# Performance work log

Hardware: AMD Instinct MI355X
Metric: run time of the kernel (lower is better)

Reference implementation:

```python
import jax, jax.numpy as jnp
import numpy as np

N = 50000      # nodes
E = 800000     # edges (avg degree 16)
IN = 256       # in_features
F1 = 32        # gnn_features per head
F2 = 32        # out_features per head
H = 8          # heads
NEG_SLOPE = 0.2


def setup_inputs() -> dict:
    key = jax.random.key(0)
    ks = jax.random.split(key, 12)
    s = 0.05
    return {
        "x":   jax.random.normal(ks[0], (N, IN), jnp.float32),
        "W1":  jax.random.normal(ks[1], (IN, H * F1), jnp.float32) * s,
        "al1": jax.random.normal(ks[2], (H, F1), jnp.float32) * s,
        "ar1": jax.random.normal(ks[3], (H, F1), jnp.float32) * s,
        "b1":  jnp.zeros((H, F1), jnp.float32),
        "W2":  jax.random.normal(ks[4], (F1, H * F2), jnp.float32) * s,
        "al2": jax.random.normal(ks[5], (H, F2), jnp.float32) * s,
        "ar2": jax.random.normal(ks[6], (H, F2), jnp.float32) * s,
        "b2":  jnp.zeros((H, F2), jnp.float32),
        "src": jax.random.randint(ks[7], (E,), 0, N, jnp.int32),
        "dst": jax.random.randint(ks[8], (E,), 0, N, jnp.int32),
    }


def _gat_layer(x, W, al, ar, b, src, dst):
    """One DGL-style GATConv. x:[N,Fin] -> [N,H,F]."""
    n, h, f = x.shape[0], al.shape[0], al.shape[1]
    z = (x @ W).reshape(n, h, f)                      # [N,H,F] projected feats
    el = jnp.einsum('nhf,hf->nh', z, al)              # src attention logits
    er = jnp.einsum('nhf,hf->nh', z, ar)              # dst attention logits
    e = el[src] + er[dst]                             # [E,H]
    e = jnp.where(e >= 0, e, NEG_SLOPE * e)           # LeakyReLU(0.2)
    # segmented (per-destination) softmax over incoming edges
    m = jax.ops.segment_max(e, dst, num_segments=n)   # [N,H]
    ex = jnp.exp(e - m[dst])                          # [E,H]
    denom = jax.ops.segment_sum(ex, dst, num_segments=n)
    alpha = ex / denom[dst]                           # [E,H]
    # weighted scatter-aggregate
    out = jax.ops.segment_sum(alpha[:, :, None] * z[src], dst, num_segments=n)
    return out + b[None]                              # [N,H,F]


def reference(x, W1, al1, ar1, b1, W2, al2, ar2, b2, src, dst):
    h = _gat_layer(x, W1, al1, ar1, b1, src, dst).mean(axis=1)   # [N,F1]
    h = jax.nn.elu(h)                                            # Dropout(0.5) = identity in eval
    out = _gat_layer(h, W2, al2, ar2, b2, src, dst).mean(axis=1) # [N,F2]
    return out
```

## Files before the change

### kernel.cpp

```cpp
#include <hip/hip_runtime.h>
#include <hip/hip_fp16.h>
#include <math.h>

#define IN_F 256
#define NHEAD 8
#define FDIM 32
#define SCAN_B 512

typedef _Float16 f16x8 __attribute__((ext_vector_type(8)));
typedef float f32x4 __attribute__((ext_vector_type(4)));

__device__ inline unsigned pkh2(float x, float y) {
  __half2 h = __floats2half2_rn(x, y);
  return *reinterpret_cast<unsigned*>(&h);
}


__global__ __launch_bounds__(256) void hist_k(const int* __restrict__ dst,
                                              int* __restrict__ deg, int E) {
  int i = blockIdx.x * 256 + threadIdx.x;
  if (i < E) atomicAdd(&deg[dst[i]], 1);
}

__global__ __launch_bounds__(SCAN_B) void scan1_k(const int* __restrict__ deg,
                                                  int* __restrict__ offs,
                                                  int* __restrict__ bsum, int N) {
  __shared__ int s[SCAN_B];
  int t = threadIdx.x;
  int i = blockIdx.x * SCAN_B + t;
  s[t] = (i < N) ? deg[i] : 0;
  __syncthreads();
  for (int off = 1; off < SCAN_B; off <<= 1) {
    int add = (t >= off) ? s[t - off] : 0;
    __syncthreads();
    s[t] += add;
    __syncthreads();
  }
  if (i < N) offs[i + 1] = s[t];
  if (t == SCAN_B - 1) bsum[blockIdx.x] = s[t];
}

__global__ __launch_bounds__(SCAN_B) void scan2_k(int* __restrict__ bsum, int nb) {
  __shared__ int s[SCAN_B];
  int t = threadIdx.x;
  s[t] = (t < nb) ? bsum[t] : 0;
  __syncthreads();
  for (int off = 1; off < SCAN_B; off <<= 1) {
    int add = (t >= off) ? s[t - off] : 0;
    __syncthreads();
    s[t] += add;
    __syncthreads();
  }
  if (t < nb) bsum[t] = (t == 0) ? 0 : s[t - 1];
}

__global__ __launch_bounds__(SCAN_B) void scan3_k(int* __restrict__ offs,
                                                  const int* __restrict__ bsum, int N) {
  int i = blockIdx.x * SCAN_B + threadIdx.x;
  if (i < N) offs[i + 1] += bsum[blockIdx.x];
  if (i == 0) offs[0] = 0;
}

__global__ __launch_bounds__(256) void scatter_k(const int* __restrict__ src,
                                                 const int* __restrict__ dst,
                                                 const int* __restrict__ offs,
                                                 int* __restrict__ cursor,
                                                 int* __restrict__ esrc, int E) {
  int i = blockIdx.x * 256 + threadIdx.x;
  if (i < E) {
    int d = dst[i];
    int pos = offs[d] + atomicAdd(&cursor[d], 1);
    esrc[pos] = src[i];
  }
}

__global__ __launch_bounds__(256) void w1cvt_k(const float* __restrict__ W1,
                                               __half* __restrict__ W1t) {
  __shared__ float s[16][17];
  int bx = blockIdx.x * 16, by = blockIdx.y * 16;
  int tx = threadIdx.x, ty = threadIdx.y;
  s[ty][tx] = W1[(by + ty) * 256 + bx + tx];
  __syncthreads();
  W1t[(size_t)(bx + ty) * 256 + by + tx] = __float2half(s[tx][ty]);
}

__global__ __launch_bounds__(256) void gemm_xw_mfma_k(const float* __restrict__ X,
                                                      const __half* __restrict__ W1t,
                                                      __half* __restrict__ Zh, int M) {
  int t = threadIdx.x;
  int wv = t >> 6, l = t & 63;
  int r = l & 15, kg = l >> 4;
  int row0 = blockIdx.x * 64 + wv * 16;
  int row = row0 + r;
  int rowc = (row < M) ? row : (M - 1);

  f16x8 a[8];
  const float* xp = X + (size_t)rowc * 256 + kg * 8;
#pragma unroll
  for (int ks = 0; ks < 8; ++ks) {
    float4 f0 = *reinterpret_cast<const float4*>(xp + ks * 32);
    float4 f1 = *reinterpret_cast<const float4*>(xp + ks * 32 + 4);
    f16x8 av;
    av[0] = (_Float16)f0.x; av[1] = (_Float16)f0.y;
    av[2] = (_Float16)f0.z; av[3] = (_Float16)f0.w;
    av[4] = (_Float16)f1.x; av[5] = (_Float16)f1.y;
    av[6] = (_Float16)f1.z; av[7] = (_Float16)f1.w;
    a[ks] = av;
  }

#pragma unroll 4
  for (int nf = 0; nf < 16; ++nf) {
    int col = nf * 16 + r;
    const f16x8* bp = reinterpret_cast<const f16x8*>(W1t + (size_t)col * 256 + kg * 8);
    f32x4 acc = {0.f, 0.f, 0.f, 0.f};
#pragma unroll
    for (int ks = 0; ks < 8; ++ks) {
      f16x8 bv = bp[ks * 4];
      acc = __builtin_amdgcn_mfma_f32_16x16x32_f16(a[ks], bv, acc, 0, 0, 0);
    }
    int orow = row0 + kg * 4;
#pragma unroll
    for (int i = 0; i < 4; ++i) {
      if (orow + i < M)
        Zh[(size_t)(orow + i) * 256 + nf * 16 + r] = __float2half((float)acc[i]);
    }
  }
}

__global__ __launch_bounds__(256) void gemm_h_k(const float* __restrict__ Hmat,
                                                const float* __restrict__ W2,
                                                __half* __restrict__ Zh, int M) {
  __shared__ float Ws[32][256];
  __shared__ float Hs[32][20];
  int t = threadIdx.x;
  for (int i = t; i < 32 * 256; i += 256) Ws[i >> 8][i & 255] = W2[i];
  int row0 = blockIdx.x * 16;
  for (int i = t; i < 16 * 32; i += 256) {
    int r = i >> 5, k = i & 31;
    Hs[k][r] = (row0 + r < M) ? Hmat[(size_t)(row0 + r) * 32 + k] : 0.f;
  }
  __syncthreads();
  int tx = t & 63, ty = t >> 6;
  float acc[4][4] = {};
#pragma unroll
  for (int k = 0; k < 32; ++k) {
    float4 a4 = *reinterpret_cast<const float4*>(&Hs[k][ty * 4]);
    float4 b4 = *reinterpret_cast<const float4*>(&Ws[k][tx * 4]);
    float a[4] = {a4.x, a4.y, a4.z, a4.w};
    float b[4] = {b4.x, b4.y, b4.z, b4.w};
#pragma unroll
    for (int i = 0; i < 4; ++i)
#pragma unroll
      for (int j = 0; j < 4; ++j) acc[i][j] = fmaf(a[i], b[j], acc[i][j]);
  }
#pragma unroll
  for (int i = 0; i < 4; ++i) {
    int r = row0 + ty * 4 + i;
    if (r < M) {
      uint2 w;
      w.x = pkh2(acc[i][0], acc[i][1]);
      w.y = pkh2(acc[i][2], acc[i][3]);
      *reinterpret_cast<uint2*>(&Zh[(size_t)r * 256 + tx * 4]) = w;
    }
  }
}

__global__ __launch_bounds__(256) void logits_k(const __half* __restrict__ Zh,
                                                const float* __restrict__ al,
                                                const float* __restrict__ ar,
                                                float* __restrict__ el,
                                                float* __restrict__ er, int N) {
  int wave = threadIdx.x >> 6;
  int lane = threadIdx.x & 63;
  int n = blockIdx.x * 4 + wave;
  if (n >= N) return;
  uint2 u = *reinterpret_cast<const uint2*>(&Zh[(size_t)n * 256 + lane * 4]);
  float2 f0 = __half22float2(*reinterpret_cast<__half2*>(&u.x));
  float2 f1 = __half22float2(*reinterpret_cast<__half2*>(&u.y));
  float4 a4 = reinterpret_cast<const float4*>(al)[lane];
  float4 r4 = reinterpret_cast<const float4*>(ar)[lane];
  float pl = f0.x * a4.x + f0.y * a4.y + f1.x * a4.z + f1.y * a4.w;
  float pr = f0.x * r4.x + f0.y * r4.y + f1.x * r4.z + f1.y * r4.w;
  pl += __shfl_xor(pl, 1); pl += __shfl_xor(pl, 2); pl += __shfl_xor(pl, 4);
  pr += __shfl_xor(pr, 1); pr += __shfl_xor(pr, 2); pr += __shfl_xor(pr, 4);
  if ((lane & 7) == 0) {
    int h = lane >> 3;
    el[(size_t)n * 8 + h] = pl;
    er[(size_t)n * 8 + h] = pr;
  }
}

__global__ __launch_bounds__(256) void alpha_k(const float* __restrict__ el,
                                               const float* __restrict__ er,
                                               const int* __restrict__ offs,
                                               const int* __restrict__ esrc,
                                               float* __restrict__ alf,
                                               float* __restrict__ rden, int N) {
  int g = blockIdx.x * 256 + threadIdx.x;
  if (g >= N * NHEAD) return;
  int n = g >> 3, h = g & 7;
  int beg = offs[n], end = offs[n + 1];
  float er_h = er[g];
  float m = -INFINITY;
  for (int i = beg; i < end; ++i) {
    float e = el[(size_t)esrc[i] * 8 + h] + er_h;
    e = (e >= 0.f) ? e : 0.2f * e;
    m = fmaxf(m, e);
  }
  float s = 0.f;
  for (int i = beg; i < end; ++i) {
    float e = el[(size_t)esrc[i] * 8 + h] + er_h;
    e = (e >= 0.f) ? e : 0.2f * e;
    float ex = __expf(e - m);
    alf[(size_t)i * 8 + h] = ex;
    s += ex;
  }
  rden[g] = (end > beg) ? 1.f / s : 0.f;
}

template <bool LAYER1>
__global__ __launch_bounds__(256) void agg_k(const __half* __restrict__ Zh,
                                             const float* __restrict__ alf,
                                             const float* __restrict__ rden,
                                             const float* __restrict__ bias,
                                             const int* __restrict__ offs,
                                             const int* __restrict__ esrc,
                                             float* __restrict__ out, int N) {
  int wid = threadIdx.x >> 6, lane = threadIdx.x & 63;
  int n = blockIdx.x * 4 + wid;
  if (n >= N) return;
  int h = lane >> 3, q = lane & 7;
  int beg = offs[n], end = offs[n + 1];
  float4 acc = make_float4(0.f, 0.f, 0.f, 0.f);
#pragma unroll 4
  for (int i = beg; i < end; ++i) {
    int sidx = esrc[i];
    float a = alf[(size_t)i * 8 + h];
    uint2 u = *reinterpret_cast<const uint2*>(&Zh[(size_t)sidx * 256 + h * 32 + q * 4]);
    float2 f0 = __half22float2(*reinterpret_cast<__half2*>(&u.x));
    float2 f1 = __half22float2(*reinterpret_cast<__half2*>(&u.y));
    acc.x = fmaf(a, f0.x, acc.x);
    acc.y = fmaf(a, f0.y, acc.y);
    acc.z = fmaf(a, f1.x, acc.z);
    acc.w = fmaf(a, f1.y, acc.w);
  }
  float r = rden[(size_t)n * 8 + h];
  float4 b4 = *reinterpret_cast<const float4*>(&bias[h * 32 + q * 4]);
  float4 v;
  v.x = fmaf(acc.x, r, b4.x);
  v.y = fmaf(acc.y, r, b4.y);
  v.z = fmaf(acc.z, r, b4.z);
  v.w = fmaf(acc.w, r, b4.w);
#pragma unroll
  for (int off = 8; off < 64; off <<= 1) {
    v.x += __shfl_xor(v.x, off);
    v.y += __shfl_xor(v.y, off);
    v.z += __shfl_xor(v.z, off);
    v.w += __shfl_xor(v.w, off);
  }
  if (h == 0) {
    v.x *= 0.125f; v.y *= 0.125f; v.z *= 0.125f; v.w *= 0.125f;
    if (LAYER1) {
      v.x = (v.x > 0.f) ? v.x : expm1f(v.x);
      v.y = (v.y > 0.f) ? v.y : expm1f(v.y);
      v.z = (v.z > 0.f) ? v.z : expm1f(v.z);
      v.w = (v.w > 0.f) ? v.w : expm1f(v.w);
    }
    *reinterpret_cast<float4*>(&out[(size_t)n * 32 + q * 4]) = v;
  }
}


extern "C" void kernel_launch(void* const* d_in, const int* in_sizes, int n_in,
                              void* d_out, int out_size, void* d_ws, size_t ws_size,
                              hipStream_t stream) {
  const float* x   = (const float*)d_in[0];
  const float* W1  = (const float*)d_in[1];
  const float* al1 = (const float*)d_in[2];
  const float* ar1 = (const float*)d_in[3];
  const float* b1  = (const float*)d_in[4];
  const float* W2  = (const float*)d_in[5];
  const float* al2 = (const float*)d_in[6];
  const float* ar2 = (const float*)d_in[7];
  const float* b2  = (const float*)d_in[8];
  const int* src   = (const int*)d_in[9];
  const int* dst   = (const int*)d_in[10];
  float* out = (float*)d_out;

  const int N = in_sizes[0] / IN_F;
  const int E = in_sizes[9];

  char* p = (char*)d_ws;
  auto alloc = [&](size_t bytes) {
    char* q = p;
    p += (bytes + 255) & ~(size_t)255;
    return q;
  };
  __half* zh  = (__half*)alloc((size_t)N * 256 * 2);
  __half* w1t = (__half*)alloc((size_t)256 * 256 * 2);
  float* el   = (float*)alloc((size_t)N * 8 * 4);
  float* er   = (float*)alloc((size_t)N * 8 * 4);
  float* h1   = (float*)alloc((size_t)N * 32 * 4);
  float* alf  = (float*)alloc((size_t)E * 8 * 4);
  float* rden = (float*)alloc((size_t)N * 8 * 4);
  int* offs   = (int*)alloc((size_t)(N + 1) * 4);
  int* deg    = (int*)alloc((size_t)N * 4);
  int* cursor = (int*)alloc((size_t)N * 4);
  int* bsum   = (int*)alloc((size_t)SCAN_B * 4);
  int* esrc   = (int*)alloc((size_t)E * 4);

  hipMemsetAsync(deg, 0, (size_t)N * 4, stream);
  hipMemsetAsync(cursor, 0, (size_t)N * 4, stream);

  int nb = (N + SCAN_B - 1) / SCAN_B;
  hist_k<<<(E + 255) / 256, 256, 0, stream>>>(dst, deg, E);
  scan1_k<<<nb, SCAN_B, 0, stream>>>(deg, offs, bsum, N);
  scan2_k<<<1, SCAN_B, 0, stream>>>(bsum, nb);
  scan3_k<<<nb, SCAN_B, 0, stream>>>(offs, bsum, N);
  scatter_k<<<(E + 255) / 256, 256, 0, stream>>>(src, dst, offs, cursor, esrc, E);

  int nh_blocks = (N * NHEAD + 255) / 256;

  w1cvt_k<<<dim3(16, 16), dim3(16, 16), 0, stream>>>(W1, w1t);
  gemm_xw_mfma_k<<<(N + 63) / 64, 256, 0, stream>>>(x, w1t, zh, N);
  logits_k<<<(N + 3) / 4, 256, 0, stream>>>(zh, al1, ar1, el, er, N);
  alpha_k<<<nh_blocks, 256, 0, stream>>>(el, er, offs, esrc, alf, rden, N);
  agg_k<true><<<(N + 3) / 4, 256, 0, stream>>>(zh, alf, rden, b1, offs, esrc, h1, N);

  gemm_h_k<<<(N + 15) / 16, 256, 0, stream>>>(h1, W2, zh, N);
  logits_k<<<(N + 3) / 4, 256, 0, stream>>>(zh, al2, ar2, el, er, N);
  alpha_k<<<nh_blocks, 256, 0, stream>>>(el, er, offs, esrc, alf, rden, N);
  agg_k<false><<<(N + 3) / 4, 256, 0, stream>>>(zh, alf, rden, b2, offs, esrc, out, N);
}
```

Baseline: 483.0 us.

## Stage W1 in swizzled LDS and compute two row tiles per wave

The X·W1 GEMM now loads the whole 256x256 fp16 W1t into a 128KB LDS buffer with an XOR swizzle. Previously each wave read B fragments straight from global memory. Each wave now handles 32 rows (two 16-row A tiles), so every B fragment is reused twice, and it splits the K accumulation into two independent chains to expose more MFMA parallelism. Blocks grow to 512 threads covering 256 rows with one block per CU. The cost is lower occupancy and a per-block 128KB LDS fill that must finish before compute starts.

```diff
diff --git a/kernel.cpp b/kernel.cpp
--- a/kernel.cpp
+++ b/kernel.cpp
@@ -84,45 +84,101 @@
   W1t[(size_t)(bx + ty) * 256 + by + tx] = __float2half(s[tx][ty]);
 }
 
-__global__ __launch_bounds__(256) void gemm_xw_mfma_k(const float* __restrict__ X,
-                                                      const __half* __restrict__ W1t,
-                                                      __half* __restrict__ Zh, int M) {
+__global__ __launch_bounds__(512, 1) void gemm_xw_mfma_k(const float* __restrict__ X,
+                                                         const __half* __restrict__ W1t,
+                                                         __half* __restrict__ Zh, int M) {
+  __shared__ __half Ws[256 * 256];
   int t = threadIdx.x;
-  int wv = t >> 6, l = t & 63;
+
+#pragma unroll
+  for (int i = 0; i < 16; ++i) {
+    int chunk = t + i * 512;
+    int col = chunk >> 5;
+    int g = chunk & 31;
+    f16x8 v = *reinterpret_cast<const f16x8*>(W1t + (size_t)col * 256 + g * 8);
+    int gs = g ^ (col & 31);
+    *reinterpret_cast<f16x8*>(&Ws[col * 256 + gs * 8]) = v;
+  }
+
+  int wid = t >> 6, l = t & 63;
   int r = l & 15, kg = l >> 4;
-  int row0 = blockIdx.x * 64 + wv * 16;
-  int row = row0 + r;
-  int rowc = (row < M) ? row : (M - 1);
-
-  f16x8 a[8];
-  const float* xp = X + (size_t)rowc * 256 + kg * 8;
+  int row0 = blockIdx.x * 256 + wid * 32;
+
+  int rowA0 = row0 + r;
+  int rowA1 = row0 + 16 + r;
+  int rc0 = (rowA0 < M) ? rowA0 : (M - 1);
+  int rc1 = (rowA1 < M) ? rowA1 : (M - 1);
+  const float* xp0 = X + (size_t)rc0 * 256 + kg * 8;
+  const float* xp1 = X + (size_t)rc1 * 256 + kg * 8;
+  f16x8 a0[8], a1[8];
 #pragma unroll
   for (int ks = 0; ks < 8; ++ks) {
-    float4 f0 = *reinterpret_cast<const float4*>(xp + ks * 32);
-    float4 f1 = *reinterpret_cast<const float4*>(xp + ks * 32 + 4);
+    float4 f0 = *reinterpret_cast<const float4*>(xp0 + ks * 32);
+    float4 f1 = *reinterpret_cast<const float4*>(xp0 + ks * 32 + 4);
     f16x8 av;
     av[0] = (_Float16)f0.x; av[1] = (_Float16)f0.y;
     av[2] = (_Float16)f0.z; av[3] = (_Float16)f0.w;
     av[4] = (_Float16)f1.x; av[5] = (_Float16)f1.y;
     av[6] = (_Float16)f1.z; av[7] = (_Float16)f1.w;
-    a[ks] = av;
-  }
-
-#pragma unroll 4
+    a0[ks] = av;
+    float4 g0 = *reinterpret_cast<const float4*>(xp1 + ks * 32);
+    float4 g1 = *reinterpret_cast<const float4*>(xp1 + ks * 32 + 4);
+    f16x8 bv;
+    bv[0] = (_Float16)g0.x; bv[1] = (_Float16)g0.y;
+    bv[2] = (_Float16)g0.z; bv[3] = (_Float16)g0.w;
+    bv[4] = (_Float16)g1.x; bv[5] = (_Float16)g1.y;
+    bv[6] = (_Float16)g1.z; bv[7] = (_Float16)g1.w;
+    a1[ks] = bv;
+  }
+
+  __syncthreads();
+
+  int orow0 = row0 + kg * 4;
+  int orow1 = row0 + 16 + kg * 4;
+
+#pragma unroll
   for (int nf = 0; nf < 16; ++nf) {
-    int col = nf * 16 + r;
-    const f16x8* bp = reinterpret_cast<const f16x8*>(W1t + (size_t)col * 256 + kg * 8);
-    f32x4 acc = {0.f, 0.f, 0.f, 0.f};
-#pragma unroll
-    for (int ks = 0; ks < 8; ++ks) {
-      f16x8 bv = bp[ks * 4];
-      acc = __builtin_amdgcn_mfma_f32_16x16x32_f16(a[ks], bv, acc, 0, 0, 0);
+    int colb = nf * 16 + r;
+    int cbase = colb * 256;
+    int cx = colb & 31;
+    f16x8 b0 = *reinterpret_cast<const f16x8*>(&Ws[cbase + ((0 * 4 + kg) ^ cx) * 8]);
+    f16x8 b1 = *reinterpret_cast<const f16x8*>(&Ws[cbase + ((1 * 4 + kg) ^ cx) * 8]);
+    f16x8 b2 = *reinterpret_cast<const f16x8*>(&Ws[cbase + ((2 * 4 + kg) ^ cx) * 8]);
+    f16x8 b3 = *reinterpret_cast<const f16x8*>(&Ws[cbase + ((3 * 4 + kg) ^ cx) * 8]);
+    f16x8 b4 = *reinterpret_cast<const f16x8*>(&Ws[cbase + ((4 * 4 + kg) ^ cx) * 8]);
+    f16x8 b5 = *reinterpret_cast<const f16x8*>(&Ws[cbase + ((5 * 4 + kg) ^ cx) * 8]);
+    f16x8 b6 = *reinterpret_cast<const f16x8*>(&Ws[cbase + ((6 * 4 + kg) ^ cx) * 8]);
+    f16x8 b7 = *reinterpret_cast<const f16x8*>(&Ws[cbase + ((7 * 4 + kg) ^ cx) * 8]);
+
+    f32x4 e0 = {0.f, 0.f, 0.f, 0.f}, e1 = {0.f, 0.f, 0.f, 0.f};
+    f32x4 f0 = {0.f, 0.f, 0.f, 0.f}, f1 = {0.f, 0.f, 0.f, 0.f};
+    e0 = __builtin_amdgcn_mfma_f32_16x16x32_f16(a0[0], b0, e0, 0, 0, 0);
+    e1 = __builtin_amdgcn_mfma_f32_16x16x32_f16(a0[1], b1, e1, 0, 0, 0);
+    f0 = __builtin_amdgcn_mfma_f32_16x16x32_f16(a1[0], b0, f0, 0, 0, 0);
+    f1 = __builtin_amdgcn_mfma_f32_16x16x32_f16(a1[1], b1, f1, 0, 0, 0);
+    e0 = __builtin_amdgcn_mfma_f32_16x16x32_f16(a0[2], b2, e0, 0, 0, 0);
+    e1 = __builtin_amdgcn_mfma_f32_16x16x32_f16(a0[3], b3, e1, 0, 0, 0);
+    f0 = __builtin_amdgcn_mfma_f32_16x16x32_f16(a1[2], b2, f0, 0, 0, 0);
+    f1 = __builtin_amdgcn_mfma_f32_16x16x32_f16(a1[3], b3, f1, 0, 0, 0);
+    e0 = __builtin_amdgcn_mfma_f32_16x16x32_f16(a0[4], b4, e0, 0, 0, 0);
+    e1 = __builtin_amdgcn_mfma_f32_16x16x32_f16(a0[5], b5, e1, 0, 0, 0);
+    f0 = __builtin_amdgcn_mfma_f32_16x16x32_f16(a1[4], b4, f0, 0, 0, 0);
+    f1 = __builtin_amdgcn_mfma_f32_16x16x32_f16(a1[5], b5, f1, 0, 0, 0);
+    e0 = __builtin_amdgcn_mfma_f32_16x16x32_f16(a0[6], b6, e0, 0, 0, 0);
+    e1 = __builtin_amdgcn_mfma_f32_16x16x32_f16(a0[7], b7, e1, 0, 0, 0);
+    f0 = __builtin_amdgcn_mfma_f32_16x16x32_f16(a1[6], b6, f0, 0, 0, 0);
+    f1 = __builtin_amdgcn_mfma_f32_16x16x32_f16(a1[7], b7, f1, 0, 0, 0);
+    f32x4 s0 = e0 + e1;
+    f32x4 s1 = f0 + f1;
+#pragma unroll
+    for (int i = 0; i < 4; ++i) {
+      if (orow0 + i < M)
+        Zh[(size_t)(orow0 + i) * 256 + nf * 16 + r] = __float2half((float)s0[i]);
     }
-    int orow = row0 + kg * 4;
 #pragma unroll
     for (int i = 0; i < 4; ++i) {
-      if (orow + i < M)
-        Zh[(size_t)(orow + i) * 256 + nf * 16 + r] = __float2half((float)acc[i]);
+      if (orow1 + i < M)
+        Zh[(size_t)(orow1 + i) * 256 + nf * 16 + r] = __float2half((float)s1[i]);
     }
   }
 }
@@ -322,7 +378,7 @@
   int nh_blocks = (N * NHEAD + 255) / 256;
 
   w1cvt_k<<<dim3(16, 16), dim3(16, 16), 0, stream>>>(W1, w1t);
-  gemm_xw_mfma_k<<<(N + 63) / 64, 256, 0, stream>>>(x, w1t, zh, N);
+  gemm_xw_mfma_k<<<(N + 255) / 256, 512, 0, stream>>>(x, w1t, zh, N);
   logits_k<<<(N + 3) / 4, 256, 0, stream>>>(zh, al1, ar1, el, er, N);
   alpha_k<<<nh_blocks, 256, 0, stream>>>(el, er, offs, esrc, alf, rden, N);
   agg_k<true><<<(N + 3) / 4, 256, 0, stream>>>(zh, alf, rden, b1, offs, esrc, h1, N);
```

Measured after the change: 439.2 us. 1.1x faster.
